# Performance work log

Measured on AMD Instinct MI355X. Metric: run time of the kernel, lower is better.

The kernel has to match this reference:

```python
import jax, jax.numpy as jnp
import numpy as np

B, C, T = 64, 128, 4096
KNOT = 4  # default knot=4 -> 6 spline knots
SIGMA = 0.2


def setup_inputs() -> dict:
    key = jax.random.key(0)
    k1, k2, k3 = jax.random.split(key, 3)
    x = jax.random.normal(k1, (B, C, T), dtype=jnp.float32)
    # yy ~ N(1.0, sigma) as in GenerateRandomCurves
    yy = 1.0 + SIGMA * jax.random.normal(k2, (B, KNOT + 2, C), dtype=jnp.float32)
    mask_rand = jax.random.uniform(k3, (B, 1, 1), dtype=jnp.float32)
    return {"x": x, "yy": yy, "mask_rand": mask_rand}


def _notaknot_matrix(n, h):
    # Moment (second-derivative) system for a not-a-knot cubic spline on a
    # uniform grid with spacing h (matches scipy.interpolate.CubicSpline default bc).
    A = np.zeros((n, n), dtype=np.float32)
    for i in range(1, n - 1):
        A[i, i - 1] = h / 6.0
        A[i, i] = 2.0 * h / 3.0
        A[i, i + 1] = h / 6.0
    # not-a-knot: third derivative continuous at x1 and x_{n-2}
    A[0, 0], A[0, 1], A[0, 2] = 1.0, -2.0, 1.0
    A[-1, -3], A[-1, -2], A[-1, -1] = 1.0, -2.0, 1.0
    return jnp.asarray(A)


def reference(x, yy, mask_rand):
    Bq, Cq, Tq = x.shape
    n = KNOT + 2
    h = (Tq - 1) / (KNOT + 1)  # uniform knot spacing; knots span [0, T-1]
    A = _notaknot_matrix(n, h)

    # Solve for spline moments M (second derivatives at knots), batched over (B, C).
    rhs_int = (yy[:, 2:, :] - 2.0 * yy[:, 1:-1, :] + yy[:, :-2, :]) / h  # (B, n-2, C)
    z = jnp.zeros((Bq, 1, Cq), yy.dtype)
    rhs = jnp.concatenate([z, rhs_int, z], axis=1)  # (B, n, C)
    M = jnp.linalg.solve(A, rhs)  # (B, n, C)

    # Evaluate the spline at t = 0..T-1 (vectorized over all batch/channel).
    tq = jnp.arange(Tq, dtype=x.dtype)
    idx = jnp.clip(jnp.floor(tq / h).astype(jnp.int32), 0, n - 2)  # (T,)
    xl = idx.astype(x.dtype) * h
    dxl = (tq - xl)[None, :, None]       # t - x_i
    dxr = (xl + h - tq)[None, :, None]   # x_{i+1} - t
    Mi, Mi1 = M[:, idx, :], M[:, idx + 1, :]      # (B, T, C)
    yi, yi1 = yy[:, idx, :], yy[:, idx + 1, :]    # (B, T, C)
    curve = ((Mi * dxr**3 + Mi1 * dxl**3) / (6.0 * h)
             + (yi / h - Mi * h / 6.0) * dxr
             + (yi1 / h - Mi1 * h / 6.0) * dxl)   # (B, T, C)

    # DistortTimesteps: cumulative sum, rescaled so the last step lands on T-1.
    tt = jnp.cumsum(curve, axis=1)
    tt = tt * (Tq - 1) / tt[:, -1:, :]  # (B, T, C)

    # Per-(batch, channel) linear interpolation back onto the regular grid.
    xp = tt.transpose(0, 2, 1).reshape(Bq * Cq, Tq)  # warped timestamps
    fp = x.reshape(Bq * Cq, Tq)                      # channel signals
    x_tw = jax.vmap(lambda a, b: jnp.interp(tq, a, b))(xp, fp)
    x_tw = x_tw.reshape(Bq, Cq, Tq)

    mask = mask_rand < 0.5  # (B,1,1): apply warp with probability p=0.5
    return jnp.where(mask, x_tw, x)
```

## Files before the change

### kernel.cpp

```cpp
#include <hip/hip_runtime.h>

#define BB 64
#define CC 128
#define TT 4096
#define NN 6
#define HH 819.0f
#define NTHR 512
#define EPT 8

__global__ __launch_bounds__(NTHR) void timewarp_kernel(
    const float* __restrict__ x,
    const float* __restrict__ yy,
    const float* __restrict__ mask_rand,
    float* __restrict__ out)
{
    const int row = blockIdx.x;
    const int b   = row / CC;
    const int c   = row % CC;
    const int tid = threadIdx.x;

    const float* xrow = x + (size_t)row * TT;
    float* orow       = out + (size_t)row * TT;

    if (!(mask_rand[b] < 0.5f)) {
        const float4* xi = (const float4*)xrow;
        float4* oo = (float4*)orow;
        oo[tid]        = xi[tid];
        oo[tid + NTHR] = xi[tid + NTHR];
        return;
    }

    __shared__ float sh_xp[TT];
    __shared__ float sh_fp[TT];
    __shared__ float sh_wsum[NTHR / 64];

    const float4 xv0 = ((const float4*)xrow)[tid];
    const float4 xv1 = ((const float4*)xrow)[tid + NTHR];

    float Mv[NN];
    float y[NN];
    {
        #pragma unroll
        for (int k = 0; k < NN; ++k)
            y[k] = yy[((size_t)b * NN + k) * CC + c];
        float Aug[NN][NN + 1];
        #pragma unroll
        for (int i = 0; i < NN; ++i)
            #pragma unroll
            for (int j = 0; j < NN + 1; ++j)
                Aug[i][j] = 0.0f;
        Aug[0][0] = 1.0f;  Aug[0][1] = -2.0f;  Aug[0][2] = 1.0f;
        Aug[5][3] = 1.0f;  Aug[5][4] = -2.0f;  Aug[5][5] = 1.0f;
        #pragma unroll
        for (int i = 1; i < NN - 1; ++i) {
            Aug[i][i - 1] = HH / 6.0f;
            Aug[i][i]     = 2.0f * HH / 3.0f;
            Aug[i][i + 1] = HH / 6.0f;
            Aug[i][NN]    = (y[i + 1] - 2.0f * y[i] + y[i - 1]) / HH;
        }
        #pragma unroll
        for (int k = 0; k < NN; ++k) {
            float inv = 1.0f / Aug[k][k];
            #pragma unroll
            for (int i = k + 1; i < NN; ++i) {
                float m = Aug[i][k] * inv;
                #pragma unroll
                for (int j = k; j < NN + 1; ++j)
                    Aug[i][j] -= m * Aug[k][j];
            }
        }
        #pragma unroll
        for (int i = NN - 1; i >= 0; --i) {
            float s = Aug[i][NN];
            #pragma unroll
            for (int j = i + 1; j < NN; ++j)
                s -= Aug[i][j] * Mv[j];
            Mv[i] = s / Aug[i][i];
        }
    }

    const int t0 = tid * EPT;
    int idxA = t0 / 819;  if (idxA > 4) idxA = 4;
    int idxB = idxA + 1;  if (idxB > 4) idxB = 4;
    float MiA = Mv[0], Mi1A = Mv[1], yiA = y[0], yi1A = y[1];
    #pragma unroll
    for (int s = 1; s <= 4; ++s)
        if (idxA >= s) { MiA = Mv[s]; Mi1A = Mv[s + 1]; yiA = y[s]; yi1A = y[s + 1]; }
    float MiB = Mv[0], Mi1B = Mv[1], yiB = y[0], yi1B = y[1];
    #pragma unroll
    for (int s = 1; s <= 4; ++s)
        if (idxB >= s) { MiB = Mv[s]; Mi1B = Mv[s + 1]; yiB = y[s]; yi1B = y[s + 1]; }
    const float tb  = (float)((idxA + 1) * 819);
    const float xlA = (float)idxA * HH;
    const float xlB = (float)idxB * HH;

    const float inv6h = 1.0f / (6.0f * HH);
    const float hd6   = HH / 6.0f;
    const float invh  = 1.0f / HH;
    float loc[EPT];
    float running = 0.0f;
    #pragma unroll
    for (int k = 0; k < EPT; ++k) {
        float ft  = (float)(t0 + k);
        bool  inB = ft >= tb;
        float Mi  = inB ? MiB  : MiA;
        float Mi1 = inB ? Mi1B : Mi1A;
        float yi  = inB ? yiB  : yiA;
        float yi1 = inB ? yi1B : yi1A;
        float xl  = inB ? xlB  : xlA;
        float dxl = ft - xl;
        float dxr = xl + HH - ft;
        float curve = (Mi * dxr * dxr * dxr + Mi1 * dxl * dxl * dxl) * inv6h
                    + (yi * invh - Mi * hd6) * dxr
                    + (yi1 * invh - Mi1 * hd6) * dxl;
        running += curve;
        loc[k] = running;
    }

    ((float4*)sh_fp)[tid]        = xv0;
    ((float4*)sh_fp)[tid + NTHR] = xv1;

    const int lane = tid & 63, wid = tid >> 6;
    float ws = running;
    #pragma unroll
    for (int d = 1; d < 64; d <<= 1) {
        float v = __shfl_up(ws, d, 64);
        if (lane >= d) ws += v;
    }
    if (lane == 63) sh_wsum[wid] = ws;
    __syncthreads();
    float wo = 0.0f, total = 0.0f;
    #pragma unroll
    for (int w = 0; w < NTHR / 64; ++w) {
        float s = sh_wsum[w];
        total += s;
        if (w < wid) wo += s;
    }
    const float offs  = wo + (ws - running);
    const float scale = 4095.0f / total;

    {
        float4 a, bq;
        a.x  = (loc[0] + offs) * scale;  a.y  = (loc[1] + offs) * scale;
        a.z  = (loc[2] + offs) * scale;  a.w  = (loc[3] + offs) * scale;
        bq.x = (loc[4] + offs) * scale;  bq.y = (loc[5] + offs) * scale;
        bq.z = (loc[6] + offs) * scale;  bq.w = (loc[7] + offs) * scale;
        ((float4*)(sh_xp + t0))[0] = a;
        ((float4*)(sh_xp + t0))[1] = bq;
    }
    __syncthreads();

    const int q0a = 4 * tid;
    const int q0b = 4 * (tid + NTHR);
    const float fq0a = (float)q0a;
    const float fq0b = (float)q0b;
    int j0 = -1, j1 = -1;
    #pragma unroll
    for (int step = 2048; step >= 1; step >>= 1) {
        int n0 = j0 + step;  n0 = (n0 > TT - 1) ? TT - 1 : n0;
        int n1 = j1 + step;  n1 = (n1 > TT - 1) ? TT - 1 : n1;
        if (sh_xp[n0] <= fq0a) j0 = n0;
        if (sh_xp[n1] <= fq0b) j1 = n1;
    }

    #pragma unroll
    for (int ch = 0; ch < 2; ++ch) {
        const int qbase = (ch == 0) ? q0a : q0b;
        int j = (ch == 0) ? j0 : j1;
        float r[4];
        #pragma unroll
        for (int e = 0; e < 4; ++e) {
            const float fq = (float)(qbase + e);
            while (j < TT - 1 && sh_xp[j + 1] <= fq) ++j;
            float v;
            if (j < 0) {
                v = sh_fp[0];
            } else if (j >= TT - 1) {
                v = sh_fp[TT - 1];
            } else {
                float xa = sh_xp[j], xb = sh_xp[j + 1];
                float fa = sh_fp[j], fb = sh_fp[j + 1];
                float d  = xb - xa;
                v = (d > 0.0f) ? fa + (fq - xa) * (fb - fa) / d : fa;
            }
            r[e] = v;
        }
        float4 res = make_float4(r[0], r[1], r[2], r[3]);
        ((float4*)orow)[tid + ch * NTHR] = res;
    }
}

extern "C" void kernel_launch(void* const* d_in, const int* in_sizes, int n_in,
                              void* d_out, int out_size, void* d_ws, size_t ws_size,
                              hipStream_t stream) {
    const float* x    = (const float*)d_in[0];
    const float* yy   = (const float*)d_in[1];
    const float* mask = (const float*)d_in[2];
    float* out = (float*)d_out;
    timewarp_kernel<<<dim3(BB * CC), dim3(NTHR), 0, stream>>>(x, yy, mask, out);
}
```

Before: 232.8 us.

## Replace binary search interpolation with scatter-built segment table and slope coefficients

Each thread now keeps its own contiguous samples and warped timestamps in registers. It precomputes per-segment intercept/slope pairs into a padded shared array and scatters segment indices into a query-to-segment table, so no binary search or linear walk is needed. The spline evaluation becomes a Horner polynomial and stores use nontemporal writes. In exchange, scatter loop lengths depend on the warp and may be unbalanced, the intercept-slope form can differ slightly from the original interpolation numerically, and the loads are now per-thread 32-byte strided rather than fully coalesced.

```diff
diff --git a/kernel.cpp b/kernel.cpp
--- a/kernel.cpp
+++ b/kernel.cpp
@@ -7,6 +7,15 @@
 #define HH 819.0f
 #define NTHR 512
 #define EPT 8
+
+typedef float f4 __attribute__((ext_vector_type(4)));
+
+__device__ __forceinline__ void nt_store4(float* p, f4 v) {
+    __builtin_nontemporal_store(v, (f4*)p);
+}
+
+__device__ __forceinline__ int p2(int j) { return j + (j >> 5); }
+#define ABSZ (4096 + 128 + 1)
 
 __global__ __launch_bounds__(NTHR) void timewarp_kernel(
     const float* __restrict__ x,
@@ -23,19 +32,27 @@
     float* orow       = out + (size_t)row * TT;
 
     if (!(mask_rand[b] < 0.5f)) {
-        const float4* xi = (const float4*)xrow;
-        float4* oo = (float4*)orow;
-        oo[tid]        = xi[tid];
-        oo[tid + NTHR] = xi[tid + NTHR];
+        const f4* xi = (const f4*)xrow;
+        nt_store4(orow + 4 * tid,            xi[tid]);
+        nt_store4(orow + 4 * (tid + NTHR),   xi[tid + NTHR]);
         return;
     }
 
-    __shared__ float sh_xp[TT];
-    __shared__ float sh_fp[TT];
-    __shared__ float sh_wsum[NTHR / 64];
-
-    const float4 xv0 = ((const float4*)xrow)[tid];
-    const float4 xv1 = ((const float4*)xrow)[tid + NTHR];
+    __shared__ float2         sh_ab[ABSZ];
+    __shared__ unsigned short sh_jt[TT];
+    __shared__ float          sh_xx[NTHR];
+    __shared__ float          sh_fx[NTHR];
+    __shared__ float          sh_wsum[NTHR / 64];
+
+    const int t0 = tid * EPT;
+    float fpv[EPT];
+    {
+        const f4 v0 = *(const f4*)(xrow + t0);
+        const f4 v1 = *(const f4*)(xrow + t0 + 4);
+        fpv[0] = v0.x; fpv[1] = v0.y; fpv[2] = v0.z; fpv[3] = v0.w;
+        fpv[4] = v1.x; fpv[5] = v1.y; fpv[6] = v1.z; fpv[7] = v1.w;
+    }
+    sh_fx[tid] = fpv[0];
 
     float Mv[NN];
     float y[NN];
@@ -79,7 +96,6 @@
         }
     }
 
-    const int t0 = tid * EPT;
     int idxA = t0 / 819;  if (idxA > 4) idxA = 4;
     int idxB = idxA + 1;  if (idxB > 4) idxB = 4;
     float MiA = Mv[0], Mi1A = Mv[1], yiA = y[0], yi1A = y[1];
@@ -90,35 +106,35 @@
     #pragma unroll
     for (int s = 1; s <= 4; ++s)
         if (idxB >= s) { MiB = Mv[s]; Mi1B = Mv[s + 1]; yiB = y[s]; yi1B = y[s + 1]; }
-    const float tb  = (float)((idxA + 1) * 819);
+    const float invh  = 1.0f / HH;
+    const float inv6h = 1.0f / (6.0f * HH);
+    const float aA = yiA;
+    const float bA = (yi1A - yiA) * invh - MiA * (HH / 3.0f) - Mi1A * (HH / 6.0f);
+    const float cA = MiA * 0.5f;
+    const float dA = (Mi1A - MiA) * inv6h;
+    const float aB = yiB;
+    const float bB = (yi1B - yiB) * invh - MiB * (HH / 3.0f) - Mi1B * (HH / 6.0f);
+    const float cB = MiB * 0.5f;
+    const float dB = (Mi1B - MiB) * inv6h;
     const float xlA = (float)idxA * HH;
     const float xlB = (float)idxB * HH;
-
-    const float inv6h = 1.0f / (6.0f * HH);
-    const float hd6   = HH / 6.0f;
-    const float invh  = 1.0f / HH;
+    const float tb  = (float)((idxA + 1) * 819);
+
     float loc[EPT];
     float running = 0.0f;
     #pragma unroll
     for (int k = 0; k < EPT; ++k) {
-        float ft  = (float)(t0 + k);
-        bool  inB = ft >= tb;
-        float Mi  = inB ? MiB  : MiA;
-        float Mi1 = inB ? Mi1B : Mi1A;
-        float yi  = inB ? yiB  : yiA;
-        float yi1 = inB ? yi1B : yi1A;
-        float xl  = inB ? xlB  : xlA;
-        float dxl = ft - xl;
-        float dxr = xl + HH - ft;
-        float curve = (Mi * dxr * dxr * dxr + Mi1 * dxl * dxl * dxl) * inv6h
-                    + (yi * invh - Mi * hd6) * dxr
-                    + (yi1 * invh - Mi1 * hd6) * dxl;
-        running += curve;
+        float ft = (float)(t0 + k);
+        bool inB = ft >= tb;
+        float xl = inB ? xlB : xlA;
+        float ca = inB ? aB : aA;
+        float cb = inB ? bB : bA;
+        float cc = inB ? cB : cA;
+        float cd = inB ? dB : dA;
+        float s  = ft - xl;
+        running += fmaf(s, fmaf(s, fmaf(s, cd, cc), cb), ca);
         loc[k] = running;
     }
-
-    ((float4*)sh_fp)[tid]        = xv0;
-    ((float4*)sh_fp)[tid + NTHR] = xv1;
 
     const int lane = tid & 63, wid = tid >> 6;
     float ws = running;
@@ -139,54 +155,60 @@
     const float offs  = wo + (ws - running);
     const float scale = 4095.0f / total;
 
-    {
-        float4 a, bq;
-        a.x  = (loc[0] + offs) * scale;  a.y  = (loc[1] + offs) * scale;
-        a.z  = (loc[2] + offs) * scale;  a.w  = (loc[3] + offs) * scale;
-        bq.x = (loc[4] + offs) * scale;  bq.y = (loc[5] + offs) * scale;
-        bq.z = (loc[6] + offs) * scale;  bq.w = (loc[7] + offs) * scale;
-        ((float4*)(sh_xp + t0))[0] = a;
-        ((float4*)(sh_xp + t0))[1] = bq;
-    }
+    float xpv[EPT + 1];
+    #pragma unroll
+    for (int k = 0; k < EPT; ++k)
+        xpv[k] = (loc[k] + offs) * scale;
+    sh_xx[tid] = xpv[0];
     __syncthreads();
-
-    const int q0a = 4 * tid;
-    const int q0b = 4 * (tid + NTHR);
-    const float fq0a = (float)q0a;
-    const float fq0b = (float)q0b;
-    int j0 = -1, j1 = -1;
-    #pragma unroll
-    for (int step = 2048; step >= 1; step >>= 1) {
-        int n0 = j0 + step;  n0 = (n0 > TT - 1) ? TT - 1 : n0;
-        int n1 = j1 + step;  n1 = (n1 > TT - 1) ? TT - 1 : n1;
-        if (sh_xp[n0] <= fq0a) j0 = n0;
-        if (sh_xp[n1] <= fq0b) j1 = n1;
-    }
+    xpv[EPT]  = (tid < NTHR - 1) ? sh_xx[tid + 1] : 4095.0f;
+    const float fpb = (tid < NTHR - 1) ? sh_fx[tid + 1] : fpv[EPT - 1];
+
+    #pragma unroll
+    for (int k = 0; k < EPT; ++k) {
+        int seg = t0 + k;
+        if (seg < TT - 1) {
+            float xa = xpv[k], xb = xpv[k + 1];
+            float fa = fpv[k];
+            float fb = (k < EPT - 1) ? fpv[k + 1] : fpb;
+            float d  = xb - xa;
+            float isl = (d > 0.0f) ? (fb - fa) * __builtin_amdgcn_rcpf(d) : 0.0f;
+            sh_ab[p2(seg)] = make_float2(fmaf(-xa, isl, fa), isl);
+            int qlo = (int)ceilf(xa);  if (qlo < 0) qlo = 0;
+            int qhi = (int)ceilf(xb);  if (qhi > TT) qhi = TT;
+            for (int q = qlo; q < qhi; ++q)
+                sh_jt[q] = (unsigned short)seg;
+        }
+    }
+    if (tid == 0) {
+        sh_ab[p2(TT - 1)] = make_float2(fpv[0], 0.0f);
+        int qh = (int)ceilf(xpv[0]);  if (qh > TT) qh = TT;
+        for (int q = 0; q < qh; ++q) sh_jt[q] = (unsigned short)(TT - 1);
+    }
+    if (tid == NTHR - 1) {
+        sh_ab[p2(TT)] = make_float2(fpv[EPT - 1], 0.0f);
+        int q0 = (int)ceilf(xpv[EPT - 1]);  if (q0 < 0) q0 = 0;
+        for (int q = q0; q < TT; ++q) sh_jt[q] = (unsigned short)TT;
+    }
+    __syncthreads();
 
     #pragma unroll
     for (int ch = 0; ch < 2; ++ch) {
-        const int qbase = (ch == 0) ? q0a : q0b;
-        int j = (ch == 0) ? j0 : j1;
-        float r[4];
-        #pragma unroll
-        for (int e = 0; e < 4; ++e) {
-            const float fq = (float)(qbase + e);
-            while (j < TT - 1 && sh_xp[j + 1] <= fq) ++j;
-            float v;
-            if (j < 0) {
-                v = sh_fp[0];
-            } else if (j >= TT - 1) {
-                v = sh_fp[TT - 1];
-            } else {
-                float xa = sh_xp[j], xb = sh_xp[j + 1];
-                float fa = sh_fp[j], fb = sh_fp[j + 1];
-                float d  = xb - xa;
-                v = (d > 0.0f) ? fa + (fq - xa) * (fb - fa) / d : fa;
-            }
-            r[e] = v;
-        }
-        float4 res = make_float4(r[0], r[1], r[2], r[3]);
-        ((float4*)orow)[tid + ch * NTHR] = res;
+        const int qb = 4 * tid + ch * (4 * NTHR);
+        ushort4 jt = *(const ushort4*)(sh_jt + qb);
+        const float fqb = (float)qb;
+        f4 res;
+        {
+            float2 s0 = sh_ab[p2((int)jt.x)];
+            float2 s1 = sh_ab[p2((int)jt.y)];
+            float2 s2 = sh_ab[p2((int)jt.z)];
+            float2 s3 = sh_ab[p2((int)jt.w)];
+            res.x = fmaf(fqb + 0.0f, s0.y, s0.x);
+            res.y = fmaf(fqb + 1.0f, s1.y, s1.x);
+            res.z = fmaf(fqb + 2.0f, s2.y, s2.x);
+            res.w = fmaf(fqb + 3.0f, s3.y, s3.x);
+        }
+        nt_store4(orow + qb, res);
     }
 }
 
```

After: 231.5 us. About the same (-0.5%).
